# Kernel optimization log

Hardware: AMD Instinct MI355X
Metric: run time of the kernel (lower is better)

The kernel has to match this reference:

```python
import jax, jax.numpy as jnp
import numpy as np

B, C, O = 8, 32, 64
G_IN, G_OUT, G_F = 33, 15, 7
X, Y, K = 64, 64, 5
INIT_ADJUST = 0.1


def setup_inputs() -> dict:
    key = jax.random.key(0)
    k1, k2, k3, k4 = jax.random.split(key, 4)
    x = jax.random.normal(k1, (B, C, G_IN, X, Y), dtype=jnp.float32)
    # idx[i, f] = in_index_dict[g_i * h_f]; per output element the G_F group
    # translates are distinct, so sample without replacement per row.
    rows = [jax.random.permutation(k, G_IN)[:G_F] for k in jax.random.split(k2, G_OUT)]
    idx = jnp.stack(rows).astype(jnp.int32)  # [G_OUT, G_F]
    weight = jax.random.normal(k3, (O, C, G_F, K, K), dtype=jnp.float32) * INIT_ADJUST
    bias = jax.random.uniform(k4, (O,), dtype=jnp.float32)
    return {"x": x, "weight": weight, "bias": bias, "idx": idx}


def reference(x, weight, bias, idx):
    # Equivalent to: scatter weight into a depth-G_IN zero kernel per output
    # group element, concat over G_OUT, run full-depth VALID conv3d.
    # Direct form: out[b,o,i,x,y] = sum_{c,f,kh,kw} x[b,c,idx[i,f],x+kh,y+kw]*W[o,c,f,kh,kw]
    b, c, g_in, xx, yy = x.shape
    o, _, g_f, kh, kw = weight.shape
    g_out = idx.shape[0]
    xg = x[:, :, idx]                                   # [B, C, G_out, G_f, X, Y]
    xg = xg.transpose(0, 2, 1, 3, 4, 5).reshape(b * g_out, c * g_f, xx, yy)
    w = weight.reshape(o, c * g_f, kh, kw)
    out = jax.lax.conv_general_dilated(
        xg, w, window_strides=(1, 1), padding="VALID",
        dimension_numbers=("NCHW", "OIHW", "NCHW"))    # [B*G_out, O, X', Y']
    out = out.reshape(b, g_out, o, xx - kh + 1, yy - kw + 1).transpose(0, 2, 1, 3, 4)
    return out + bias[None, :, None, None, None]
```

## Files before the change

kernel.cpp:

```cpp
#include <hip/hip_runtime.h>
#include <hip/hip_bf16.h>

#define GF    7
#define TAPS  25
#define NCHNK 7
#define NTILE 10
#define TROWS 6
#define SROWS 10
#define NPOS  360
#define NF_   23

typedef __attribute__((ext_vector_type(8)))  __bf16 bf16x8;
typedef __attribute__((ext_vector_type(8)))  unsigned short u16x8;
typedef __attribute__((ext_vector_type(4)))  float f32x4;

__device__ __forceinline__ f32x4 mfma16(u16x8 a, u16x8 b, f32x4 c) {
  return __builtin_amdgcn_mfma_f32_16x16x32_bf16(
      __builtin_bit_cast(bf16x8, a), __builtin_bit_cast(bf16x8, b), c, 0, 0, 0);
}

__device__ __forceinline__ void glds16(const unsigned short* g, unsigned short* l) {
  __builtin_amdgcn_global_load_lds(
      (__attribute__((address_space(1))) void*)g,
      (__attribute__((address_space(3))) void*)l, 16, 0, 0);
}

__global__ void wt_kernel(const float* __restrict__ w, unsigned short* __restrict__ wt) {
  int i = blockIdx.x * 256 + threadIdx.x;
  if (i >= NCHNK * TAPS * 64 * 32) return;
  int c   = i & 31;
  int o   = (i >> 5) & 63;
  int tap = (i >> 11) % TAPS;
  int ck  = i / (TAPS * 64 * 32);
  float v = w[((size_t)(o * 32 + c) * GF + ck) * TAPS + tap];
  __bf16 hb = (__bf16)v;
  wt[i] = __builtin_bit_cast(unsigned short, hb);
}

__global__ void xt_kernel(const float* __restrict__ x, unsigned short* __restrict__ xt) {
  int blk = blockIdx.x;
  int row = blk & 63;
  int pl  = blk >> 6;
  int tid = threadIdx.x;
  int col = tid >> 2, oct = tid & 3;
  int b = pl / 33, gin = pl - 33 * b;
  const float* xp = x + (((size_t)b * 32 * 33 + gin) << 12) + row * 64 + col;
  u16x8 pk;
#pragma unroll
  for (int e = 0; e < 8; ++e) {
    float v = xp[(size_t)(8 * oct + e) * 135168];
    pk[e] = __builtin_bit_cast(unsigned short, (__bf16)v);
  }
  int pos = row * 64 + col;
  *reinterpret_cast<u16x8*>(
      &xt[((size_t)pl << 17) + pos * 32 + 8 * (oct ^ ((pos >> 1) & 3))]) = pk;
}

__global__ void __launch_bounds__(256, 2)
conv_kernel(const unsigned short* __restrict__ xt, const unsigned short* __restrict__ wt,
            const float* __restrict__ bias, const int* __restrict__ idx,
            float* __restrict__ out) {
  __shared__ __align__(16) unsigned short Xs[640 * 32];

  const int bid0 = blockIdx.x;
  const int bid  = (bid0 & 7) * 150 + (bid0 >> 3);
  const int tile = bid % NTILE;
  const int g    = (bid / NTILE) % 15;
  const int b    = bid / (NTILE * 15);

  const int tid  = threadIdx.x;
  const int lane = tid & 63;
  const int wv   = tid >> 6;
  const int lo   = lane & 15;
  const int lk   = lane >> 4;
  const int r0   = tile * TROWS;

  int g7[NCHNK];
#pragma unroll
  for (int f = 0; f < NCHNK; ++f) g7[f] = idx[g * GF + f];

  auto issue_xs = [&](int ckp) {
    const unsigned short* src =
        xt + (((size_t)(b * 33 + g7[ckp])) << 17) + r0 * 2048 + wv * 5120 + lane * 8;
#pragma unroll
    for (int t = 0; t < 10; ++t)
      glds16(src + t * 512, Xs + wv * 5120 + t * 512);
  };

  const int alane = lo * 32 + lk * 8;
  auto load_a = [&](u16x8* dst, int ck, int tap) {
    const unsigned short* p = wt + ((ck * TAPS + tap) << 11) + alane;
#pragma unroll
    for (int m = 0; m < 4; ++m)
      dst[m] = *reinterpret_cast<const u16x8*>(p + m * 512);
  };

  int pb5[6][5];
  int pvalid = 0;
#pragma unroll
  for (int i = 0; i < 6; ++i) {
    int nf = wv + 4 * i;
#pragma unroll
    for (int kw = 0; kw < 5; ++kw) pb5[i][kw] = 8 * lk;
    if (nf < NF_) {
      int p  = nf * 16 + lo;
      int pc = (p < NPOS) ? p : 0;
      int ph = pc / 60;
      int pos0 = ph * 64 + (pc - 60 * ph);
#pragma unroll
      for (int kw = 0; kw < 5; ++kw) {
        int ptk = pos0 + kw;
        pb5[i][kw] = ptk * 32 + 8 * (lk ^ ((ptk >> 1) & 3));
      }
      pvalid = i + 1;
    }
  }

  f32x4 acc[4][6];
#pragma unroll
  for (int m = 0; m < 4; ++m)
#pragma unroll
    for (int i = 0; i < 6; ++i) acc[m][i] = f32x4{0.f, 0.f, 0.f, 0.f};

  u16x8 aE[4], aO[4];
  load_a(aE, 0, 0);
  issue_xs(0);
  asm volatile("s_waitcnt vmcnt(0) lgkmcnt(0)" ::: "memory");
  __builtin_amdgcn_s_barrier();

#pragma unroll 1
  for (int ck = 0; ck < NCHNK; ++ck) {
#pragma unroll
    for (int kh = 0; kh < 5; ++kh) {
#pragma unroll
      for (int kw = 0; kw < 5; ++kw) {
        const int tap = kh * 5 + kw;
        u16x8* aCur = (tap & 1) ? aO : aE;
        u16x8* aNxt = (tap & 1) ? aE : aO;
        if (tap < 24) load_a(aNxt, ck, tap + 1);
        u16x8 bf[6];
#pragma unroll
        for (int i = 0; i < 6; ++i)
          if (i < pvalid)
            bf[i] = *reinterpret_cast<const u16x8*>(&Xs[pb5[i][kw] + kh * 2048]);
#pragma unroll
        for (int i = 0; i < 6; ++i)
          if (i < pvalid)
#pragma unroll
            for (int m = 0; m < 4; ++m)
              acc[m][i] = mfma16(aCur[m], bf[i], acc[m][i]);
        if (tap == 24 && ck + 1 < NCHNK)
          load_a(aE, ck + 1, 0);
      }
    }
    if (ck + 1 < NCHNK) {
      __builtin_amdgcn_s_barrier();
      issue_xs(ck + 1);
      asm volatile("s_waitcnt vmcnt(0)" ::: "memory");
      __builtin_amdgcn_s_barrier();
    }
  }

  float bv[4][4];
#pragma unroll
  for (int m = 0; m < 4; ++m)
#pragma unroll
    for (int v = 0; v < 4; ++v) bv[m][v] = bias[m * 16 + 4 * lk + v];

#pragma unroll
  for (int i = 0; i < 6; ++i) {
    if (i < pvalid) {
      int nf = wv + 4 * i;
      int p  = nf * 16 + lo;
      if (p < NPOS) {
        const size_t pb = (size_t)tile * NPOS + p;
#pragma unroll
        for (int m = 0; m < 4; ++m)
#pragma unroll
          for (int v = 0; v < 4; ++v) {
            int o = m * 16 + 4 * lk + v;
            out[((size_t)(b * 64 + o) * 15 + g) * 3600 + pb] = acc[m][i][v] + bv[m][v];
          }
      }
    }
  }
}

extern "C" void kernel_launch(void* const* d_in, const int* in_sizes, int n_in,
                              void* d_out, int out_size, void* d_ws, size_t ws_size,
                              hipStream_t stream) {
  const float* x      = (const float*)d_in[0];
  const float* weight = (const float*)d_in[1];
  const float* bias   = (const float*)d_in[2];
  const int*   idx    = (const int*)d_in[3];
  float* out = (float*)d_out;
  unsigned short* wt = (unsigned short*)d_ws;
  unsigned short* xt = (unsigned short*)d_ws + 358400;

  wt_kernel<<<(NCHNK * TAPS * 64 * 32 + 255) / 256, 256, 0, stream>>>(weight, wt);
  xt_kernel<<<264 * 64, 256, 0, stream>>>(x, xt);
  conv_kernel<<<8 * 15 * NTILE, 256, 0, stream>>>(xt, wt, bias, idx, out);
}
```

Before: 302.8 us.

## Map waves to 2D row/column tiles and raise conv occupancy to three blocks

Output positions are no longer assigned as flattened 16-wide fragments (23 fragments spread unevenly across 4 waves). Each wave now owns a 16-column strip across all 6 tile rows, so the LDS B-fragment address is just a per-kw offset plus a row stride. This removes the 6x5 per-fragment address table and the validity branches, freeing registers, and the launch bound is raised so three blocks can share a CU. In exchange, 4 of the 64 computed columns fall outside the 60 valid ones, adding a little wasted MFMA work. The shared buffer is padded by 4 rows so those overrun reads stay inside allocated LDS.

```diff
diff --git a/kernel.cpp b/kernel.cpp
--- a/kernel.cpp
+++ b/kernel.cpp
@@ -7,8 +7,6 @@
 #define NTILE 10
 #define TROWS 6
 #define SROWS 10
-#define NPOS  360
-#define NF_   23
 
 typedef __attribute__((ext_vector_type(8)))  __bf16 bf16x8;
 typedef __attribute__((ext_vector_type(8)))  unsigned short u16x8;
@@ -56,11 +54,11 @@
       &xt[((size_t)pl << 17) + pos * 32 + 8 * (oct ^ ((pos >> 1) & 3))]) = pk;
 }
 
-__global__ void __launch_bounds__(256, 2)
+__global__ void __launch_bounds__(256, 3)
 conv_kernel(const unsigned short* __restrict__ xt, const unsigned short* __restrict__ wt,
             const float* __restrict__ bias, const int* __restrict__ idx,
             float* __restrict__ out) {
-  __shared__ __align__(16) unsigned short Xs[640 * 32];
+  __shared__ __align__(16) unsigned short Xs[644 * 32];
 
   const int bid0 = blockIdx.x;
   const int bid  = (bid0 & 7) * 150 + (bid0 >> 3);
@@ -95,25 +93,11 @@
       dst[m] = *reinterpret_cast<const u16x8*>(p + m * 512);
   };
 
-  int pb5[6][5];
-  int pvalid = 0;
+  int pbk[5];
 #pragma unroll
-  for (int i = 0; i < 6; ++i) {
-    int nf = wv + 4 * i;
-#pragma unroll
-    for (int kw = 0; kw < 5; ++kw) pb5[i][kw] = 8 * lk;
-    if (nf < NF_) {
-      int p  = nf * 16 + lo;
-      int pc = (p < NPOS) ? p : 0;
-      int ph = pc / 60;
-      int pos0 = ph * 64 + (pc - 60 * ph);
-#pragma unroll
-      for (int kw = 0; kw < 5; ++kw) {
-        int ptk = pos0 + kw;
-        pb5[i][kw] = ptk * 32 + 8 * (lk ^ ((ptk >> 1) & 3));
-      }
-      pvalid = i + 1;
-    }
+  for (int kw = 0; kw < 5; ++kw) {
+    int cw = wv * 16 + lo + kw;
+    pbk[kw] = cw * 32 + 8 * (lk ^ ((cw >> 1) & 3));
   }
 
   f32x4 acc[4][6];
@@ -141,14 +125,12 @@
         u16x8 bf[6];
 #pragma unroll
         for (int i = 0; i < 6; ++i)
-          if (i < pvalid)
-            bf[i] = *reinterpret_cast<const u16x8*>(&Xs[pb5[i][kw] + kh * 2048]);
+          bf[i] = *reinterpret_cast<const u16x8*>(&Xs[pbk[kw] + (i + kh) * 2048]);
 #pragma unroll
         for (int i = 0; i < 6; ++i)
-          if (i < pvalid)
 #pragma unroll
-            for (int m = 0; m < 4; ++m)
-              acc[m][i] = mfma16(aCur[m], bf[i], acc[m][i]);
+          for (int m = 0; m < 4; ++m)
+            acc[m][i] = mfma16(aCur[m], bf[i], acc[m][i]);
         if (tap == 24 && ck + 1 < NCHNK)
           load_a(aE, ck + 1, 0);
       }
@@ -167,21 +149,18 @@
 #pragma unroll
     for (int v = 0; v < 4; ++v) bv[m][v] = bias[m * 16 + 4 * lk + v];
 
+  const int colo = wv * 16 + lo;
+  if (colo < 60) {
 #pragma unroll
-  for (int i = 0; i < 6; ++i) {
-    if (i < pvalid) {
-      int nf = wv + 4 * i;
-      int p  = nf * 16 + lo;
-      if (p < NPOS) {
-        const size_t pb = (size_t)tile * NPOS + p;
+    for (int i = 0; i < 6; ++i) {
+      const size_t pb = (size_t)(r0 + i) * 60 + colo;
 #pragma unroll
-        for (int m = 0; m < 4; ++m)
+      for (int m = 0; m < 4; ++m)
 #pragma unroll
-          for (int v = 0; v < 4; ++v) {
-            int o = m * 16 + 4 * lk + v;
-            out[((size_t)(b * 64 + o) * 15 + g) * 3600 + pb] = acc[m][i][v] + bv[m][v];
-          }
-      }
+        for (int v = 0; v < 4; ++v) {
+          int o = m * 16 + 4 * lk + v;
+          out[((size_t)(b * 64 + o) * 15 + g) * 3600 + pb] = acc[m][i][v] + bv[m][v];
+        }
     }
   }
 }
```

Result: slower. 752.4 us (+148.5%).
